# Kernel optimization log

Hardware: AMD Instinct MI355X
Metric: run time of the kernel (lower is better)

The kernel has to match this reference:

```python
import jax, jax.numpy as jnp
import numpy as np

N = 4_000_000   # number of (parent, child) edges
N_RELS = 20
P = 3            # n_polarities
Z_EPS = 0.01
COS_EPS = 0.01
SCALE_FACTOR = 42.0


def setup_inputs() -> dict:
    key = jax.random.key(0)
    k1, k2, k3, k4, k5, k6, k7 = jax.random.split(key, 7)
    child_probs = jax.random.uniform(k1, (N, P), dtype=jnp.float32)
    prnt_probs = jax.random.uniform(k2, (N, P), dtype=jnp.float32)
    child_probs = child_probs * (jax.random.uniform(k3, (N, 1)) > 0.1).astype(jnp.float32)
    prnt_probs = prnt_probs * (jax.random.uniform(k4, (N, 1)) > 0.1).astype(jnp.float32)
    rels = jax.random.randint(k5, (N,), 0, N_RELS)
    eps_M = jax.random.normal(k6, (N, P, P), dtype=jnp.float32)
    beta = jax.random.beta(k7, 15.0, 15.0, (N,), dtype=jnp.float32)  # Beta(beta_p, beta_q), all 15.0
    # learned/fixed params per __init__
    MU = np.eye(P, dtype=np.float32)
    MU[1, :] = [-0.25, 0.5, -0.25]
    rel_mu = jnp.asarray(np.tile(MU, (N_RELS, 1)).reshape(N_RELS, P, P))
    rel_sigma = jnp.ones((N_RELS, P, P), dtype=jnp.float32)
    return {"prnt_probs": prnt_probs, "child_probs": child_probs, "rel_mu": rel_mu,
            "rel_sigma": rel_sigma, "eps_M": eps_M, "beta": beta, "rels": rels}


def _safe_norm(x):
    sq = jnp.sum(x * x, axis=-1)
    return jnp.where(sq == 0.0, 0.0, jnp.sqrt(jnp.where(sq == 0.0, 1.0, sq)))


def _scale(prnt, child):
    # z = max(eps, p + c); normalize; entropy; cosine similarity; scale = 42 * cos / H(z)
    z = jnp.maximum(Z_EPS, prnt + child)
    z = z / jnp.sum(z, axis=-1, keepdims=True)
    entropy = -jnp.sum(z * jnp.log(z), axis=-1)
    cos = jnp.sum(prnt * child, axis=-1)
    norm = _safe_norm(prnt) * _safe_norm(child)
    norm = jnp.where(norm == 0.0, 1.0, norm)
    cos = jnp.maximum(COS_EPS, cos / norm)
    return SCALE_FACTOR * cos / entropy


def reference(prnt_probs, child_probs, rel_mu, rel_sigma, eps_M, beta, rels):
    # mask-based equivalent of the nonzero()-gather version (static shapes for jit)
    child_mask = jnp.sum(child_probs, axis=-1) != 0.0          # rows with nonzero child probs
    # M ~ Normal(mu[rels], sigma[rels]) reparameterized
    M = rel_mu[rels] + rel_sigma[rels] * eps_M                  # [N, P, P]
    cp = jax.nn.softmax(jnp.einsum('nij,nj->ni', M, child_probs), axis=-1)  # [N, P]
    prnt_sum = jnp.sum(prnt_probs, axis=-1)
    copy_mask = child_mask & (prnt_sum == 0.0)                  # child copied to parent
    alpha_mask = child_mask & (prnt_sum != 0.0)                 # blended update
    s = _scale(prnt_probs, cp)                                  # [N]
    alpha = ((1.0 - beta)[:, None] * prnt_probs + beta[:, None] * cp) * s[:, None]
    child_probs2copy = jnp.where(copy_mask[:, None], cp, 0.0)
    alpha = jnp.where(alpha_mask[:, None], alpha, 0.0)
    return copy_mask, child_probs2copy, alpha_mask, alpha
```

## Files before the change

### kernel.cpp

```cpp
#include <hip/hip_runtime.h>

#define BLOCK 256
#define RPT   4
#define RPB   (BLOCK * RPT)

__device__ __forceinline__ void row_compute(
    const float* p, const float* c, const float* e,
    float bb, int rq,
    const float* smu, const float* ssg,
    float* o1, float* o3, float& m0v, float& m2v)
{
    const float* mu = &smu[9 * rq];
    const float* sg = &ssg[9 * rq];

    float l[3];
    #pragma unroll
    for (int i = 0; i < 3; ++i) {
        float acc = 0.0f;
        #pragma unroll
        for (int j = 0; j < 3; ++j) {
            float m = fmaf(sg[3 * i + j], e[3 * i + j], mu[3 * i + j]);
            acc = fmaf(m, c[j], acc);
        }
        l[i] = acc;
    }
    float mx = fmaxf(l[0], fmaxf(l[1], l[2]));
    float e0 = __expf(l[0] - mx), e1 = __expf(l[1] - mx), e2 = __expf(l[2] - mx);
    float einv = 1.0f / (e0 + e1 + e2);
    float cp0 = e0 * einv, cp1 = e1 * einv, cp2 = e2 * einv;

    float csum = c[0] + c[1] + c[2];
    float psum = p[0] + p[1] + p[2];
    bool cmask = (csum != 0.0f);
    bool copy  = cmask && (psum == 0.0f);
    bool amask = cmask && (psum != 0.0f);

    float z0 = fmaxf(0.01f, p[0] + cp0);
    float z1 = fmaxf(0.01f, p[1] + cp1);
    float z2 = fmaxf(0.01f, p[2] + cp2);
    float zinv = 1.0f / (z0 + z1 + z2);
    z0 *= zinv; z1 *= zinv; z2 *= zinv;
    float ent = -(z0 * __logf(z0) + z1 * __logf(z1) + z2 * __logf(z2));
    float cosv = p[0] * cp0 + p[1] * cp1 + p[2] * cp2;
    float np2 = p[0] * p[0] + p[1] * p[1] + p[2] * p[2];
    float nc2 = cp0 * cp0 + cp1 * cp1 + cp2 * cp2;
    float npn = (np2 == 0.0f) ? 0.0f : sqrtf(np2);
    float ncn = (nc2 == 0.0f) ? 0.0f : sqrtf(nc2);
    float nrm = npn * ncn;
    nrm = (nrm == 0.0f) ? 1.0f : nrm;
    cosv = fmaxf(0.01f, cosv / nrm);
    float s = 42.0f * cosv / ent;

    float ob = 1.0f - bb;
    float a0 = fmaf(ob, p[0], bb * cp0) * s;
    float a1 = fmaf(ob, p[1], bb * cp1) * s;
    float a2 = fmaf(ob, p[2], bb * cp2) * s;

    m0v = copy  ? 1.0f : 0.0f;
    m2v = amask ? 1.0f : 0.0f;
    o1[0] = copy ? cp0 : 0.0f;
    o1[1] = copy ? cp1 : 0.0f;
    o1[2] = copy ? cp2 : 0.0f;
    o3[0] = amask ? a0 : 0.0f;
    o3[1] = amask ? a1 : 0.0f;
    o3[2] = amask ? a2 : 0.0f;
}

__global__ __launch_bounds__(BLOCK, 2) void alpha_kernel(
    const float* __restrict__ prnt,
    const float* __restrict__ child,
    const float* __restrict__ rel_mu,
    const float* __restrict__ rel_sigma,
    const float* __restrict__ eps,
    const float* __restrict__ beta,
    const int*  __restrict__ rels,
    float* __restrict__ out0,
    float* __restrict__ out1,
    float* __restrict__ out2,
    float* __restrict__ out3,
    int n_rows, int nmu)
{
    __shared__ float smu[192];
    __shared__ float ssg[192];

    const int tid = threadIdx.x;
    if (tid < nmu) { smu[tid] = rel_mu[tid]; ssg[tid] = rel_sigma[tid]; }
    __syncthreads();

    const long T  = (long)blockIdx.x * BLOCK + tid;
    const long r0 = T * RPT;
    if (r0 >= n_rows) return;

    if (r0 + RPT <= n_rows) {
        const float4* p4 = (const float4*)prnt;
        const float4* c4 = (const float4*)child;
        const float4* e4 = (const float4*)eps;
        const float4* b4 = (const float4*)beta;
        const int4*   r4 = (const int4*)rels;

        float4 P[3], C[3], E[9];
        #pragma unroll
        for (int k = 0; k < 3; ++k) P[k] = p4[3 * T + k];
        #pragma unroll
        for (int k = 0; k < 3; ++k) C[k] = c4[3 * T + k];
        #pragma unroll
        for (int k = 0; k < 9; ++k) E[k] = e4[9 * T + k];
        float4 bt = b4[T];
        int4   rl = r4[T];

        const float* Pf = (const float*)P;
        const float* Cf = (const float*)C;
        const float* Ef = (const float*)E;
        float bq[RPT] = {bt.x, bt.y, bt.z, bt.w};
        int   rq[RPT] = {rl.x, rl.y, rl.z, rl.w};

        float o1[12], o3[12], m0[RPT], m2[RPT];
        #pragma unroll
        for (int r = 0; r < RPT; ++r) {
            row_compute(Pf + 3 * r, Cf + 3 * r, Ef + 9 * r,
                        bq[r], rq[r], smu, ssg,
                        o1 + 3 * r, o3 + 3 * r, m0[r], m2[r]);
        }

        ((float4*)out0)[T] = make_float4(m0[0], m0[1], m0[2], m0[3]);
        ((float4*)out2)[T] = make_float4(m2[0], m2[1], m2[2], m2[3]);
        float4* o1g = (float4*)out1;
        float4* o3g = (float4*)out3;
        const float4* o1l = (const float4*)o1;
        const float4* o3l = (const float4*)o3;
        #pragma unroll
        for (int k = 0; k < 3; ++k) o1g[3 * T + k] = o1l[k];
        #pragma unroll
        for (int k = 0; k < 3; ++k) o3g[3 * T + k] = o3l[k];
    } else {
        for (long r = r0; r < n_rows; ++r) {
            float p[3], c[3], e[9];
            #pragma unroll
            for (int k = 0; k < 3; ++k) p[k] = prnt[3 * r + k];
            #pragma unroll
            for (int k = 0; k < 3; ++k) c[k] = child[3 * r + k];
            #pragma unroll
            for (int k = 0; k < 9; ++k) e[k] = eps[9 * r + k];
            float o1s[3], o3s[3], m0s, m2s;
            row_compute(p, c, e, beta[r], rels[r], smu, ssg, o1s, o3s, m0s, m2s);
            out0[r] = m0s;
            out2[r] = m2s;
            #pragma unroll
            for (int k = 0; k < 3; ++k) out1[3 * r + k] = o1s[k];
            #pragma unroll
            for (int k = 0; k < 3; ++k) out3[3 * r + k] = o3s[k];
        }
    }
}

extern "C" void kernel_launch(void* const* d_in, const int* in_sizes, int n_in,
                              void* d_out, int out_size, void* d_ws, size_t ws_size,
                              hipStream_t stream)
{
    const float* prnt      = (const float*)d_in[0];
    const float* child     = (const float*)d_in[1];
    const float* rel_mu    = (const float*)d_in[2];
    const float* rel_sigma = (const float*)d_in[3];
    const float* eps       = (const float*)d_in[4];
    const float* beta      = (const float*)d_in[5];
    const int*   rels      = (const int*)d_in[6];

    const int N   = in_sizes[5];
    const int nmu = in_sizes[2];

    float* out  = (float*)d_out;
    float* out0 = out;
    float* out1 = out + (size_t)N;
    float* out2 = out + (size_t)4 * N;
    float* out3 = out + (size_t)5 * N;

    int blocks = (N + RPB - 1) / RPB;
    alpha_kernel<<<blocks, BLOCK, 0, stream>>>(
        prnt, child, rel_mu, rel_sigma, eps, beta, rels,
        out0, out1, out2, out3, N, nmu);
}
```

Measured before the change: 355.5 us.

## Persistent blocks with double-buffered async LDS staging and coalesced stores

Replaces the per-thread 4-row float4 loads with a persistent-block loop over 256-row tiles. Each tile is prefetched into a double-buffered LDS area using global_load_lds async copies while the current tile is computed. Outputs for the vector results are staged through LDS and written as coalesced float2 stores, with hand-placed waitcnt barriers. This aims to increase memory-level parallelism and coalescing, at the cost of LDS pressure, fragile manual waitcnt accounting and a capped grid size.

```diff
diff --git a/kernel.cpp b/kernel.cpp
--- a/kernel.cpp
+++ b/kernel.cpp
@@ -1,8 +1,28 @@
 #include <hip/hip_runtime.h>
 
 #define BLOCK 256
-#define RPT   4
-#define RPB   (BLOCK * RPT)
+#define TILE  256
+#define GBLK  1024
+
+typedef const __attribute__((address_space(1))) void* gas1_t;
+typedef __attribute__((address_space(3)))       void* las3_t;
+
+__device__ __forceinline__ void ld_lds16(const float4* g, float4* l) {
+    __builtin_amdgcn_global_load_lds((gas1_t)(const void*)g, (las3_t)(void*)l, 16, 0, 0);
+}
+
+__device__ __forceinline__ void bar_lgkm0() {
+    asm volatile("s_waitcnt lgkmcnt(0)" ::: "memory");
+    __builtin_amdgcn_sched_barrier(0);
+    __builtin_amdgcn_s_barrier();
+    __builtin_amdgcn_sched_barrier(0);
+}
+__device__ __forceinline__ void bar_vm5_lgkm0() {
+    asm volatile("s_waitcnt vmcnt(5) lgkmcnt(0)" ::: "memory");
+    __builtin_amdgcn_sched_barrier(0);
+    __builtin_amdgcn_s_barrier();
+    __builtin_amdgcn_sched_barrier(0);
+}
 
 __device__ __forceinline__ void row_compute(
     const float* p, const float* c, const float* e,
@@ -66,90 +86,149 @@
     o3[2] = amask ? a2 : 0.0f;
 }
 
-__global__ __launch_bounds__(BLOCK, 2) void alpha_kernel(
-    const float* __restrict__ prnt,
-    const float* __restrict__ child,
-    const float* __restrict__ rel_mu,
-    const float* __restrict__ rel_sigma,
-    const float* __restrict__ eps,
-    const float* __restrict__ beta,
-    const int*  __restrict__ rels,
+__global__ __launch_bounds__(BLOCK, 3) void alpha_kernel(
+    const float4* __restrict__ prnt4,
+    const float4* __restrict__ child4,
+    const float*  __restrict__ rel_mu,
+    const float*  __restrict__ rel_sigma,
+    const float4* __restrict__ eps4,
+    const float4* __restrict__ beta4,
+    const float4* __restrict__ rels4,
     float* __restrict__ out0,
     float* __restrict__ out1,
     float* __restrict__ out2,
     float* __restrict__ out3,
     int n_rows, int nmu)
 {
-    __shared__ float smu[192];
-    __shared__ float ssg[192];
-
-    const int tid = threadIdx.x;
+    __shared__ float4 s_p[2][192];
+    __shared__ float4 s_c[2][192];
+    __shared__ float4 s_e[2][576];
+    __shared__ float4 s_b[2][64];
+    __shared__ float4 s_r[2][64];
+    __shared__ float  s_ob[1536];
+    __shared__ float  smu[192], ssg[192];
+
+    const int tid  = threadIdx.x;
+    const int lane = tid & 63;
+    const int wv   = tid >> 6;
+    const int nt   = (n_rows + TILE - 1) / TILE;
+    const int G    = (int)gridDim.x;
+
     if (tid < nmu) { smu[tid] = rel_mu[tid]; ssg[tid] = rel_sigma[tid]; }
+
+    auto stage = [&](int t, int bb) {
+        const int rows = min(TILE, n_rows - t * TILE);
+        if (rows == TILE) {
+            const float4* gp = prnt4  + (size_t)t * 192;
+            const float4* gc = child4 + (size_t)t * 192;
+            const float4* ge = eps4   + (size_t)t * 576;
+            const float4* gb = beta4  + (size_t)t * 64;
+            const float4* gr = rels4  + (size_t)t * 64;
+            for (int ch = wv; ch < 17; ch += 4) {
+                if      (ch < 3)  ld_lds16(gp + ch * 64 + lane,       &s_p[bb][ch * 64]);
+                else if (ch < 6)  ld_lds16(gc + (ch - 3) * 64 + lane, &s_c[bb][(ch - 3) * 64]);
+                else if (ch < 15) ld_lds16(ge + (ch - 6) * 64 + lane, &s_e[bb][(ch - 6) * 64]);
+                else if (ch == 15) ld_lds16(gb + lane, &s_b[bb][0]);
+                else               ld_lds16(gr + lane, &s_r[bb][0]);
+            }
+        } else {
+            const float* gpf = (const float*)prnt4;
+            const float* gcf = (const float*)child4;
+            const float* gef = (const float*)eps4;
+            const float* gbf = (const float*)beta4;
+            const int*   gri = (const int*)rels4;
+            for (int i = tid; i < rows * 3; i += BLOCK) {
+                ((float*)&s_p[bb][0])[i] = gpf[(size_t)t * 768 + i];
+                ((float*)&s_c[bb][0])[i] = gcf[(size_t)t * 768 + i];
+            }
+            for (int i = tid; i < rows * 9; i += BLOCK)
+                ((float*)&s_e[bb][0])[i] = gef[(size_t)t * 2304 + i];
+            for (int i = tid; i < rows; i += BLOCK) {
+                ((float*)&s_b[bb][0])[i] = gbf[(size_t)t * 256 + i];
+                ((int*)&s_r[bb][0])[i]   = gri[(size_t)t * 256 + i];
+            }
+        }
+    };
+
+    int t = blockIdx.x;
+    int cur = 0;
+    if (t < nt) stage(t, 0);
     __syncthreads();
 
-    const long T  = (long)blockIdx.x * BLOCK + tid;
-    const long r0 = T * RPT;
-    if (r0 >= n_rows) return;
-
-    if (r0 + RPT <= n_rows) {
-        const float4* p4 = (const float4*)prnt;
-        const float4* c4 = (const float4*)child;
-        const float4* e4 = (const float4*)eps;
-        const float4* b4 = (const float4*)beta;
-        const int4*   r4 = (const int4*)rels;
-
-        float4 P[3], C[3], E[9];
-        #pragma unroll
-        for (int k = 0; k < 3; ++k) P[k] = p4[3 * T + k];
-        #pragma unroll
-        for (int k = 0; k < 3; ++k) C[k] = c4[3 * T + k];
-        #pragma unroll
-        for (int k = 0; k < 9; ++k) E[k] = e4[9 * T + k];
-        float4 bt = b4[T];
-        int4   rl = r4[T];
-
-        const float* Pf = (const float*)P;
-        const float* Cf = (const float*)C;
-        const float* Ef = (const float*)E;
-        float bq[RPT] = {bt.x, bt.y, bt.z, bt.w};
-        int   rq[RPT] = {rl.x, rl.y, rl.z, rl.w};
-
-        float o1[12], o3[12], m0[RPT], m2[RPT];
-        #pragma unroll
-        for (int r = 0; r < RPT; ++r) {
-            row_compute(Pf + 3 * r, Cf + 3 * r, Ef + 9 * r,
-                        bq[r], rq[r], smu, ssg,
-                        o1 + 3 * r, o3 + 3 * r, m0[r], m2[r]);
+    while (t < nt) {
+        const int nxt = t + G;
+        if (nxt < nt) stage(nxt, cur ^ 1);
+
+        const int rows_here = min(TILE, n_rows - t * TILE);
+        if (rows_here == TILE) {
+            const float* pf = (const float*)&s_p[cur][0];
+            const float* cf = (const float*)&s_c[cur][0];
+            const float* ef = (const float*)&s_e[cur][0];
+            float p[3], c[3], e[9];
+            #pragma unroll
+            for (int k = 0; k < 3; ++k) p[k] = pf[3 * tid + k];
+            #pragma unroll
+            for (int k = 0; k < 3; ++k) c[k] = cf[3 * tid + k];
+            #pragma unroll
+            for (int k = 0; k < 9; ++k) e[k] = ef[9 * tid + k];
+            const float bb = ((const float*)&s_b[cur][0])[tid];
+            const int   rq = ((const int*)&s_r[cur][0])[tid];
+
+            float o1[3], o3[3], m0, m2;
+            row_compute(p, c, e, bb, rq, smu, ssg, o1, o3, m0, m2);
+
+            out0[(size_t)t * 256 + tid] = m0;
+            out2[(size_t)t * 256 + tid] = m2;
+
+            #pragma unroll
+            for (int k = 0; k < 3; ++k) s_ob[3 * tid + k]       = o1[k];
+            #pragma unroll
+            for (int k = 0; k < 3; ++k) s_ob[768 + 3 * tid + k] = o3[k];
+
+            bar_lgkm0();
+
+            const float2* ob2 = (const float2*)s_ob;
+            float2* o1g = (float2*)out1 + (size_t)t * 384;
+            float2* o3g = (float2*)out3 + (size_t)t * 384;
+            #pragma unroll
+            for (int j = 0; j < 3; ++j) {
+                const int i = tid + 256 * j;
+                float2 v = ob2[i];
+                float2* dst = (i < 384) ? (o1g + i) : (o3g + (i - 384));
+                *dst = v;
+            }
+
+            bar_vm5_lgkm0();
+        } else {
+            const bool act = tid < rows_here;
+            if (act) {
+                const size_t r = (size_t)t * 256 + tid;
+                const float* gpf = (const float*)prnt4;
+                const float* gcf = (const float*)child4;
+                const float* gef = (const float*)eps4;
+                float p[3], c[3], e[9];
+                #pragma unroll
+                for (int k = 0; k < 3; ++k) p[k] = gpf[3 * r + k];
+                #pragma unroll
+                for (int k = 0; k < 3; ++k) c[k] = gcf[3 * r + k];
+                #pragma unroll
+                for (int k = 0; k < 9; ++k) e[k] = gef[9 * r + k];
+                const float bb = ((const float*)beta4)[r];
+                const int   rq = ((const int*)rels4)[r];
+                float o1[3], o3[3], m0, m2;
+                row_compute(p, c, e, bb, rq, smu, ssg, o1, o3, m0, m2);
+                out0[r] = m0;
+                out2[r] = m2;
+                #pragma unroll
+                for (int k = 0; k < 3; ++k) out1[3 * r + k] = o1[k];
+                #pragma unroll
+                for (int k = 0; k < 3; ++k) out3[3 * r + k] = o3[k];
+            }
+            __syncthreads();
         }
 
-        ((float4*)out0)[T] = make_float4(m0[0], m0[1], m0[2], m0[3]);
-        ((float4*)out2)[T] = make_float4(m2[0], m2[1], m2[2], m2[3]);
-        float4* o1g = (float4*)out1;
-        float4* o3g = (float4*)out3;
-        const float4* o1l = (const float4*)o1;
-        const float4* o3l = (const float4*)o3;
-        #pragma unroll
-        for (int k = 0; k < 3; ++k) o1g[3 * T + k] = o1l[k];
-        #pragma unroll
-        for (int k = 0; k < 3; ++k) o3g[3 * T + k] = o3l[k];
-    } else {
-        for (long r = r0; r < n_rows; ++r) {
-            float p[3], c[3], e[9];
-            #pragma unroll
-            for (int k = 0; k < 3; ++k) p[k] = prnt[3 * r + k];
-            #pragma unroll
-            for (int k = 0; k < 3; ++k) c[k] = child[3 * r + k];
-            #pragma unroll
-            for (int k = 0; k < 9; ++k) e[k] = eps[9 * r + k];
-            float o1s[3], o3s[3], m0s, m2s;
-            row_compute(p, c, e, beta[r], rels[r], smu, ssg, o1s, o3s, m0s, m2s);
-            out0[r] = m0s;
-            out2[r] = m2s;
-            #pragma unroll
-            for (int k = 0; k < 3; ++k) out1[3 * r + k] = o1s[k];
-            #pragma unroll
-            for (int k = 0; k < 3; ++k) out3[3 * r + k] = o3s[k];
-        }
+        cur ^= 1;
+        t = nxt;
     }
 }
 
@@ -174,8 +253,10 @@
     float* out2 = out + (size_t)4 * N;
     float* out3 = out + (size_t)5 * N;
 
-    int blocks = (N + RPB - 1) / RPB;
+    const int nt = (N + TILE - 1) / TILE;
+    const int blocks = nt < GBLK ? nt : GBLK;
     alpha_kernel<<<blocks, BLOCK, 0, stream>>>(
-        prnt, child, rel_mu, rel_sigma, eps, beta, rels,
+        (const float4*)prnt, (const float4*)child, rel_mu, rel_sigma,
+        (const float4*)eps, (const float4*)beta, (const float4*)rels,
         out0, out1, out2, out3, N, nmu);
 }
```

Result: faster. 341.2 us (-4.0%).

## Stage row tiles into LDS with async global_load_lds double buffering per wave

Applied to the files above, without the earlier changes.

Replaces the one-thread-four-rows register load scheme with a persistent per-wave loop. Each wave streams 64-row tiles directly into LDS using global_load_lds, double-buffered with explicit vmcnt waits, and writes outputs back through LDS so the stores are coalesced. The goal is to keep more loads in flight and avoid strided per-thread vector loads in this memory-bound kernel. It adds hand-counted waitcnt logic that must match the number of issued loads, and LDS bank conflicts on the stride-3 and stride-9 reads.

```diff
diff --git a/kernel.cpp b/kernel.cpp
--- a/kernel.cpp
+++ b/kernel.cpp
@@ -1,18 +1,27 @@
 #include <hip/hip_runtime.h>
 
 #define BLOCK 256
-#define RPT   4
-#define RPB   (BLOCK * RPT)
+#define WPB   4
+#define TROWS 64
+#define TF4   272
+
+typedef const __attribute__((address_space(1))) void* gas1_t;
+typedef __attribute__((address_space(3)))       void* las3_t;
+
+__device__ __forceinline__ void ld_lds16(const float4* g, float4* l) {
+    __builtin_amdgcn_global_load_lds((gas1_t)(const void*)g, (las3_t)(void*)l, 16, 0, 0);
+}
+
+#define WAITV(N) do { asm volatile("s_waitcnt vmcnt(" #N ")" ::: "memory"); \
+                      __builtin_amdgcn_sched_barrier(0); } while (0)
 
 __device__ __forceinline__ void row_compute(
     const float* p, const float* c, const float* e,
-    float bb, int rq,
-    const float* smu, const float* ssg,
+    float bb, int rq, const float* smu, const float* ssg,
     float* o1, float* o3, float& m0v, float& m2v)
 {
     const float* mu = &smu[9 * rq];
     const float* sg = &ssg[9 * rq];
-
     float l[3];
     #pragma unroll
     for (int i = 0; i < 3; ++i) {
@@ -66,89 +75,125 @@
     o3[2] = amask ? a2 : 0.0f;
 }
 
-__global__ __launch_bounds__(BLOCK, 2) void alpha_kernel(
-    const float* __restrict__ prnt,
-    const float* __restrict__ child,
-    const float* __restrict__ rel_mu,
-    const float* __restrict__ rel_sigma,
-    const float* __restrict__ eps,
-    const float* __restrict__ beta,
-    const int*  __restrict__ rels,
-    float* __restrict__ out0,
-    float* __restrict__ out1,
-    float* __restrict__ out2,
-    float* __restrict__ out3,
+__global__ __launch_bounds__(BLOCK, 4) void alpha_kernel(
+    const float4* __restrict__ prnt4,
+    const float4* __restrict__ child4,
+    const float*  __restrict__ rel_mu,
+    const float*  __restrict__ rel_sigma,
+    const float4* __restrict__ eps4,
+    const float4* __restrict__ beta4,
+    const float4* __restrict__ rels4,
+    float*  __restrict__ out0,
+    float4* __restrict__ out1f4,
+    float*  __restrict__ out2,
+    float4* __restrict__ out3f4,
     int n_rows, int nmu)
 {
-    __shared__ float smu[192];
-    __shared__ float ssg[192];
-
-    const int tid = threadIdx.x;
+    __shared__ float4 s_tiles[WPB][2][TF4];
+    __shared__ float  smu[192], ssg[192];
+
+    const int tid  = threadIdx.x;
+    const int lane = tid & 63;
+    const int wv   = tid >> 6;
+
     if (tid < nmu) { smu[tid] = rel_mu[tid]; ssg[tid] = rel_sigma[tid]; }
     __syncthreads();
 
-    const long T  = (long)blockIdx.x * BLOCK + tid;
-    const long r0 = T * RPT;
-    if (r0 >= n_rows) return;
-
-    if (r0 + RPT <= n_rows) {
-        const float4* p4 = (const float4*)prnt;
-        const float4* c4 = (const float4*)child;
-        const float4* e4 = (const float4*)eps;
-        const float4* b4 = (const float4*)beta;
-        const int4*   r4 = (const int4*)rels;
-
-        float4 P[3], C[3], E[9];
-        #pragma unroll
-        for (int k = 0; k < 3; ++k) P[k] = p4[3 * T + k];
-        #pragma unroll
-        for (int k = 0; k < 3; ++k) C[k] = c4[3 * T + k];
-        #pragma unroll
-        for (int k = 0; k < 9; ++k) E[k] = e4[9 * T + k];
-        float4 bt = b4[T];
-        int4   rl = r4[T];
-
-        const float* Pf = (const float*)P;
-        const float* Cf = (const float*)C;
-        const float* Ef = (const float*)E;
-        float bq[RPT] = {bt.x, bt.y, bt.z, bt.w};
-        int   rq[RPT] = {rl.x, rl.y, rl.z, rl.w};
-
-        float o1[12], o3[12], m0[RPT], m2[RPT];
-        #pragma unroll
-        for (int r = 0; r < RPT; ++r) {
-            row_compute(Pf + 3 * r, Cf + 3 * r, Ef + 9 * r,
-                        bq[r], rq[r], smu, ssg,
-                        o1 + 3 * r, o3 + 3 * r, m0[r], m2[r]);
-        }
-
-        ((float4*)out0)[T] = make_float4(m0[0], m0[1], m0[2], m0[3]);
-        ((float4*)out2)[T] = make_float4(m2[0], m2[1], m2[2], m2[3]);
-        float4* o1g = (float4*)out1;
-        float4* o3g = (float4*)out3;
-        const float4* o1l = (const float4*)o1;
-        const float4* o3l = (const float4*)o3;
-        #pragma unroll
-        for (int k = 0; k < 3; ++k) o1g[3 * T + k] = o1l[k];
-        #pragma unroll
-        for (int k = 0; k < 3; ++k) o3g[3 * T + k] = o3l[k];
-    } else {
-        for (long r = r0; r < n_rows; ++r) {
+    const long ntf   = n_rows / TROWS;
+    const long wgid  = (long)blockIdx.x * WPB + wv;
+    const long W     = (long)gridDim.x * WPB;
+    const long nmine = (wgid < ntf) ? ((ntf - 1 - wgid) / W + 1) : 0;
+
+    auto stage = [&](long t, int b) {
+        float4* dst = &s_tiles[wv][b][0];
+        const float4* gp = prnt4  + t * 48;
+        const float4* gc = child4 + t * 48;
+        const float4* ge = eps4   + t * 144;
+        const float4* gb = beta4  + t * 16;
+        const float4* gr = rels4  + t * 16;
+        ld_lds16(ge + lane,      dst + 96);
+        ld_lds16(ge + 64 + lane, dst + 160);
+        if (lane < 48) {
+            ld_lds16(gp + lane, dst + 0);
+            ld_lds16(gc + lane, dst + 48);
+        }
+        if (lane < 16) {
+            ld_lds16(ge + 128 + lane, dst + 224);
+            ld_lds16(gb + lane,       dst + 240);
+            ld_lds16(gr + lane,       dst + 256);
+        }
+    };
+
+    if (nmine >= 1) stage(wgid, 0);
+    if (nmine >= 2) stage(wgid + W, 1);
+
+    long k = wgid;
+    int  b = 0;
+    for (long i = 0; i < nmine; ++i, k += W, b ^= 1) {
+        const bool more = (i + 1 < nmine);
+        const bool prev = (i > 0);
+        if      (more && prev) { WAITV(11); }
+        else if (more)         { WAITV(7);  }
+        else if (prev)         { WAITV(4);  }
+        else                   { WAITV(0);  }
+
+        float* fw = (float*)&s_tiles[wv][b][0];
+        const float* f = fw;
+        float p[3], c[3], e[9];
+        #pragma unroll
+        for (int q = 0; q < 3; ++q) p[q] = f[3 * lane + q];
+        #pragma unroll
+        for (int q = 0; q < 3; ++q) c[q] = f[192 + 3 * lane + q];
+        #pragma unroll
+        for (int q = 0; q < 9; ++q) e[q] = f[384 + 9 * lane + q];
+        const float bt = f[960 + lane];
+        const int   rq = ((const int*)fw)[1024 + lane];
+
+        float o1[3], o3[3], m0, m2;
+        row_compute(p, c, e, bt, rq, smu, ssg, o1, o3, m0, m2);
+
+        #pragma unroll
+        for (int q = 0; q < 3; ++q) fw[3 * lane + q]       = o1[q];
+        #pragma unroll
+        for (int q = 0; q < 3; ++q) fw[192 + 3 * lane + q] = o3[q];
+
+        out0[k * 64 + lane] = m0;
+        out2[k * 64 + lane] = m2;
+        const float4* bf = (const float4*)fw;
+        if (lane < 48) {
+            out1f4[k * 48 + lane] = bf[lane];
+            out3f4[k * 48 + lane] = bf[48 + lane];
+        }
+
+        if (i + 2 < nmine) stage(k + 2 * W, b);
+    }
+
+    const long rem = ntf * TROWS;
+    if (rem < n_rows && wgid == 0) {
+        const long r = rem + lane;
+        if (r < n_rows) {
+            const float* gpf = (const float*)prnt4;
+            const float* gcf = (const float*)child4;
+            const float* gef = (const float*)eps4;
             float p[3], c[3], e[9];
             #pragma unroll
-            for (int k = 0; k < 3; ++k) p[k] = prnt[3 * r + k];
-            #pragma unroll
-            for (int k = 0; k < 3; ++k) c[k] = child[3 * r + k];
-            #pragma unroll
-            for (int k = 0; k < 9; ++k) e[k] = eps[9 * r + k];
-            float o1s[3], o3s[3], m0s, m2s;
-            row_compute(p, c, e, beta[r], rels[r], smu, ssg, o1s, o3s, m0s, m2s);
-            out0[r] = m0s;
-            out2[r] = m2s;
-            #pragma unroll
-            for (int k = 0; k < 3; ++k) out1[3 * r + k] = o1s[k];
-            #pragma unroll
-            for (int k = 0; k < 3; ++k) out3[3 * r + k] = o3s[k];
+            for (int q = 0; q < 3; ++q) p[q] = gpf[3 * r + q];
+            #pragma unroll
+            for (int q = 0; q < 3; ++q) c[q] = gcf[3 * r + q];
+            #pragma unroll
+            for (int q = 0; q < 9; ++q) e[q] = gef[9 * r + q];
+            const float bt = ((const float*)beta4)[r];
+            const int   rq = ((const int*)rels4)[r];
+            float o1[3], o3[3], m0, m2;
+            row_compute(p, c, e, bt, rq, smu, ssg, o1, o3, m0, m2);
+            out0[r] = m0;
+            out2[r] = m2;
+            float* o1f = (float*)out1f4;
+            float* o3f = (float*)out3f4;
+            #pragma unroll
+            for (int q = 0; q < 3; ++q) o1f[3 * r + q] = o1[q];
+            #pragma unroll
+            for (int q = 0; q < 3; ++q) o3f[3 * r + q] = o3[q];
         }
     }
 }
@@ -174,8 +219,14 @@
     float* out2 = out + (size_t)4 * N;
     float* out3 = out + (size_t)5 * N;
 
-    int blocks = (N + RPB - 1) / RPB;
+    int blocks = 1024;
+    const long ntf = (long)N / TROWS;
+    if (ntf < (long)blocks * WPB) blocks = (int)((ntf + WPB - 1) / WPB);
+    if (blocks < 1) blocks = 1;
+
     alpha_kernel<<<blocks, BLOCK, 0, stream>>>(
-        prnt, child, rel_mu, rel_sigma, eps, beta, rels,
-        out0, out1, out2, out3, N, nmu);
-}
+        (const float4*)prnt, (const float4*)child, rel_mu, rel_sigma,
+        (const float4*)eps, (const float4*)beta, (const float4*)rels,
+        out0, (float4*)out1, out2, (float4*)out3,
+        N, nmu);
+}
```

New measurement: 336.6 us. 5.3% less time.
